# Optimization experiments

Measured on AMD Instinct MI355X. Metric: run time of the kernel, lower is better.

## Reference

```python
import jax, jax.numpy as jnp
import numpy as np

B, N, E = 32, 2048, 4096
D_IN, C, H = 256, 64, 4          # node_hidden_size, gnn_hidden_size, num_heads
SLOPE = 0.2                       # PyG GATConv default negative_slope


def gat_conv(x, src, dst, W, att_src, att_dst, bias):
    """One PyG-style GATConv (concat=True, add_self_loops=True) on a single graph.
    x: [N, Din]; src/dst: [E] int; W: [Din, H*C]; att_*: [H, C]; bias: [H*C]."""
    n = x.shape[0]
    h = (x @ W).reshape(n, H, C)                       # [N,H,C]
    a_src = jnp.einsum('nhc,hc->nh', h, att_src)       # [N,H]
    a_dst = jnp.einsum('nhc,hc->nh', h, att_dst)
    loop = jnp.arange(n, dtype=src.dtype)              # self loops
    s = jnp.concatenate([src, loop])
    d = jnp.concatenate([dst, loop])
    e = jax.nn.leaky_relu(a_src[s] + a_dst[d], SLOPE)  # [E+N,H]
    # segment softmax over incoming edges of each target node
    m = jax.ops.segment_max(e, d, num_segments=n)
    ex = jnp.exp(e - m[d])
    denom = jax.ops.segment_sum(ex, d, num_segments=n)
    alpha = ex / (denom[d] + 1e-16)                    # [E+N,H]
    out = jax.ops.segment_sum(alpha[:, :, None] * h[s], d, num_segments=n)  # [N,H,C]
    return out.reshape(n, H * C) + bias


def setup_inputs() -> dict:
    key = jax.random.key(0)
    ks = jax.random.split(key, 12)
    g = lambda k, shp, fan: jax.random.normal(k, shp, jnp.float32) * (1.0 / np.sqrt(fan))
    return {
        'node_embeddings': jax.random.normal(ks[0], (B, N, D_IN), jnp.float32),
        'src_index': jax.random.randint(ks[1], (B, E), 0, N, jnp.int32),
        'tgt_index': jax.random.randint(ks[2], (B, E), 0, N, jnp.int32),
        'W1': g(ks[3], (D_IN, H * C), D_IN),
        'att_src1': g(ks[4], (H, C), C),
        'att_dst1': g(ks[5], (H, C), C),
        'bias1': jnp.zeros((H * C,), jnp.float32),
        'W2': g(ks[6], (H * C, H * C), H * C),
        'att_src2': g(ks[7], (H, C), C),
        'att_dst2': g(ks[8], (H, C), C),
        'bias2': jnp.zeros((H * C,), jnp.float32),
    }


def reference(node_embeddings, src_index, tgt_index, W1, att_src1, att_dst1, bias1,
              W2, att_src2, att_dst2, bias2):
    def per_graph(x, s, d):
        m = gat_conv(x, s, d, W1, att_src1, att_dst1, bias1)
        m = jax.nn.elu(m)                              # dropout = identity (eval)
        m = gat_conv(m, s, d, W2, att_src2, att_dst2, bias2)
        return m
    return jax.vmap(per_graph)(node_embeddings, src_index, tgt_index)  # [B,N,H*C]
```

## Files before the change

kernel.cpp:

```cpp
#include <hip/hip_runtime.h>
#include <hip/hip_bf16.h>
#include <cstdint>

#define BB 32
#define NN 2048
#define EE 4096
#define HH 4
#define CC 64
#define DD 256
#define MM (BB*NN)

typedef __attribute__((ext_vector_type(8))) short bf16x8;
typedef __attribute__((ext_vector_type(4))) float f32x4;

__device__ __forceinline__ float b2f(__hip_bfloat16 x){ return __bfloat162float(x); }
__device__ __forceinline__ float u2f(unsigned short u){ return __uint_as_float((unsigned)u << 16); }
__device__ __forceinline__ unsigned short f2u(float f){
  __hip_bfloat16 h = __float2bfloat16(f);
  return *(unsigned short*)&h;
}
__device__ __forceinline__ float ldany(const void* p, int isf, size_t i){
  return isf ? ((const float*)p)[i] : b2f(((const __hip_bfloat16*)p)[i]);
}
__device__ __forceinline__ void gld_lds16(const void* g, void* l){
  __builtin_amdgcn_global_load_lds((const __attribute__((address_space(1))) uint32_t*)g,
                                   (__attribute__((address_space(3))) uint32_t*)l, 16, 0, 0);
}

__global__ void detect_kernel(const unsigned* __restrict__ w, int* __restrict__ flag){
  __shared__ int cnt;
  if(threadIdx.x == 0) cnt = 0;
  __syncthreads();
  int c = 0;
  #pragma unroll
  for(int i = 0; i < 4; ++i){
    unsigned v = w[threadIdx.x*4 + i];
    unsigned elo = (v >> 7) & 0xFFu;
    if(elo >= 100u && elo <= 150u) ++c;
  }
  atomicAdd(&cnt, c);
  __syncthreads();
  if(threadIdx.x == 0) *flag = (cnt < 128) ? 1 : 0;
}

__global__ __launch_bounds__(256) void convX_kernel(const void* __restrict__ src,
    unsigned short* __restrict__ dst, const int* __restrict__ flag){
  int isf = *flag;
  size_t i = ((size_t)blockIdx.x*256 + threadIdx.x)*4;
  ushort4 o;
  if(isf){
    float4 v = *(const float4*)((const float*)src + i);
    o.x = f2u(v.x); o.y = f2u(v.y); o.z = f2u(v.z); o.w = f2u(v.w);
  } else {
    o = *(const ushort4*)((const unsigned short*)src + i);
  }
  *(ushort4*)(dst + i) = o;
}
__global__ __launch_bounds__(256) void convWT_kernel(const void* __restrict__ W,
    __hip_bfloat16* __restrict__ WT, const int* __restrict__ flag){
  int isf = *flag;
  int i = blockIdx.x*256 + threadIdx.x;
  WT[i] = __float2bfloat16(ldany(W, isf, (size_t)(i & 255)*256 + (i >> 8)));
}
__global__ __launch_bounds__(256) void conv6_kernel(const void* s0, const void* s1,
    const void* s2, const void* s3, const void* s4, const void* s5,
    float* __restrict__ dst, const int* __restrict__ flag){
  int isf = *flag;
  int i = blockIdx.x*256 + threadIdx.x;
  int seg = i >> 8, off = i & 255;
  const void* s = seg==0?s0 : seg==1?s1 : seg==2?s2 : seg==3?s3 : seg==4?s4 : s5;
  dst[i] = ldany(s, isf, off);
}

__global__ __launch_bounds__(256) void mfma_gemm(const __hip_bfloat16* __restrict__ A,
    const __hip_bfloat16* __restrict__ BT, __hip_bfloat16* __restrict__ C,
    const float* __restrict__ attS, const float* __restrict__ attD,
    float* __restrict__ aS, float* __restrict__ aD)
{
  __shared__ __align__(16) short lA[128*64];
  __shared__ __align__(16) short lB[128*64];
  const int tid  = threadIdx.x;
  const int w    = tid >> 6, lane = tid & 63;
  const int row0 = blockIdx.x*128, col0 = blockIdx.y*128;
  const int wr   = (w & 1)*64, wc = (w >> 1)*64;
  const int lr   = lane >> 3;
  const int kb_g = (lane & 7) ^ lr;
  const int fm   = lane & 15, quad = lane >> 4;
  f32x4 acc[4][4] = {};

  for(int k0 = 0; k0 < 256; k0 += 64){
    #pragma unroll
    for(int c = 0; c < 4; ++c){
      int ra = w*32 + c*8;
      const short* ga = (const short*)A  + (size_t)(row0 + ra + lr)*DD + k0 + kb_g*8;
      const short* gb = (const short*)BT + (size_t)(col0 + ra + lr)*DD + k0 + kb_g*8;
      gld_lds16(ga, &lA[ra*64]);
      gld_lds16(gb, &lB[ra*64]);
    }
    __syncthreads();
    #pragma unroll
    for(int ks = 0; ks < 2; ++ks){
      bf16x8 af[4], bfr[4];
      int kb = ks*4 + quad;
      #pragma unroll
      for(int i = 0; i < 4; ++i){
        int m = wr + i*16 + fm;
        af[i]  = *(const bf16x8*)&lA[m*64 + ((kb ^ (m & 7))*8)];
        int n = wc + i*16 + fm;
        bfr[i] = *(const bf16x8*)&lB[n*64 + ((kb ^ (n & 7))*8)];
      }
      #pragma unroll
      for(int i = 0; i < 4; ++i)
        #pragma unroll
        for(int j = 0; j < 4; ++j)
          acc[i][j] = __builtin_amdgcn_mfma_f32_16x16x32_bf16(af[i], bfr[j], acc[i][j], 0, 0, 0);
    }
    __syncthreads();
  }

  #pragma unroll
  for(int i = 0; i < 4; ++i)
    #pragma unroll
    for(int j = 0; j < 4; ++j)
      #pragma unroll
      for(int r = 0; r < 4; ++r){
        int row = row0 + wr + i*16 + quad*4 + r;
        int col = col0 + wc + j*16 + fm;
        C[(size_t)row*DD + col] = __float2bfloat16(acc[i][j][r]);
      }

  const int headI = (col0 + wc) >> 6;
  float ws_[4], wd_[4];
  #pragma unroll
  for(int j = 0; j < 4; ++j){
    ws_[j] = attS[headI*CC + j*16 + fm];
    wd_[j] = attD[headI*CC + j*16 + fm];
  }
  #pragma unroll
  for(int i = 0; i < 4; ++i){
    #pragma unroll
    for(int r = 0; r < 4; ++r){
      float s = 0.f, dv = 0.f;
      #pragma unroll
      for(int j = 0; j < 4; ++j){
        float v = acc[i][j][r];
        s  += v * ws_[j];
        dv += v * wd_[j];
      }
      #pragma unroll
      for(int m = 1; m <= 8; m <<= 1){
        s  += __shfl_xor(s,  m);
        dv += __shfl_xor(dv, m);
      }
      if(fm == i*4 + r){
        int row = row0 + wr + i*16 + quad*4 + r;
        aS[(size_t)row*HH + headI] = s;
        aD[(size_t)row*HH + headI] = dv;
      }
    }
  }
}

__global__ __launch_bounds__(256) void deg_kernel(const int* __restrict__ dst, int* __restrict__ degc)
{
  int idx = blockIdx.x*256 + threadIdx.x;
  if(idx >= BB*EE) return;
  int b = idx >> 12;
  atomicAdd(&degc[b*NN + dst[idx]], 1);
}

__global__ __launch_bounds__(256) void scan_kernel(int* __restrict__ degc, int* __restrict__ row_ptr)
{
  __shared__ int part[256];
  int b = blockIdx.x, t = threadIdx.x;
  int loc[8], s = 0;
  #pragma unroll
  for(int i = 0; i < 8; ++i){ loc[i] = s; s += degc[b*NN + t*8 + i]; }
  part[t] = s;
  __syncthreads();
  if(t == 0){
    int run = 0;
    for(int i = 0; i < 256; ++i){ int tmp = part[i]; part[i] = run; run += tmp; }
  }
  __syncthreads();
  int base = b*EE + part[t];
  #pragma unroll
  for(int i = 0; i < 8; ++i){
    int v = base + loc[i];
    row_ptr[b*(NN+1) + t*8 + i] = v;
    degc   [b*NN     + t*8 + i] = v;
  }
  if(t == 255) row_ptr[b*(NN+1) + NN] = base + s;
}

__global__ __launch_bounds__(256) void scatter_kernel(const int* __restrict__ src,
    const int* __restrict__ dst, int* __restrict__ cursor, unsigned short* __restrict__ srcList)
{
  int idx = blockIdx.x*256 + threadIdx.x;
  if(idx >= BB*EE) return;
  int b = idx >> 12;
  int pos = atomicAdd(&cursor[b*NN + dst[idx]], 1);
  srcList[pos] = (unsigned short)src[idx];
}

__global__ __launch_bounds__(256) void alpha_kernel(const float* __restrict__ a_src,
    const float* __restrict__ a_dst, const int* __restrict__ row_ptr,
    const unsigned short* __restrict__ srcList, float* __restrict__ alpha,
    float* __restrict__ alphaSelf, float* __restrict__ denG)
{
  int idx = blockIdx.x*256 + threadIdx.x;
  if(idx >= MM*HH) return;
  int h  = idx & (HH-1);
  int bn = idx >> 2;
  int b  = bn >> 11;
  int d  = bn & (NN-1);
  int start = row_ptr[b*(NN+1) + d];
  int end   = row_ptr[b*(NN+1) + d + 1];
  float adv  = a_dst[idx];
  float self = a_src[idx] + adv;
  self = self > 0.f ? self : 0.2f*self;
  float exs = __expf(self), den = exs;
  for(int e = start; e < end; ++e){
    int s = srcList[e];
    float v = a_src[(b*NN + s)*HH + h] + adv;
    v = v > 0.f ? v : 0.2f*v;
    float ex = __expf(v);
    alpha[e*HH + h] = ex;
    den += ex;
  }
  alphaSelf[idx] = exs;
  denG[idx] = den;
}

template<int LAYER>
__global__ __launch_bounds__(256) void gather_kernel(const __hip_bfloat16* __restrict__ H,
    const float* __restrict__ alpha, const float* __restrict__ alphaSelf,
    const float* __restrict__ denG,
    const int* __restrict__ row_ptr, const unsigned short* __restrict__ srcList,
    const float* __restrict__ bias, void* __restrict__ outp,
    const int* __restrict__ flag)
{
  int wid  = (int)(((size_t)blockIdx.x*256 + threadIdx.x) >> 6);
  int lane = threadIdx.x & 63;
  if(wid >= MM) return;
  int b = wid >> 11, d = wid & (NN-1);
  int head = lane >> 4;
  int start = row_ptr[b*(NN+1) + d];
  int end   = row_ptr[b*(NN+1) + d + 1];
  const unsigned short* Hu = (const unsigned short*)H;

  float aS   = alphaSelf[wid*HH + head];
  float denv = denG[wid*HH + head];
  ushort4 hv = *(const ushort4*)(Hu + (size_t)wid*DD + lane*4);
  f32x4 acc;
  acc.x = aS*u2f(hv.x); acc.y = aS*u2f(hv.y); acc.z = aS*u2f(hv.z); acc.w = aS*u2f(hv.w);

  int e = start;
  int s  = 0; float a = 0.f;
  if(e < end){ s = srcList[e]; a = alpha[e*HH + head]; }
  while(e < end){
    int   sn = 0; float an = 0.f;
    if(e + 1 < end){ sn = srcList[e+1]; an = alpha[(e+1)*HH + head]; }
    ushort4 v = *(const ushort4*)(Hu + (size_t)(b*NN + s)*DD + lane*4);
    acc.x += a*u2f(v.x); acc.y += a*u2f(v.y); acc.z += a*u2f(v.z); acc.w += a*u2f(v.w);
    s = sn; a = an; ++e;
  }
  float inv = 1.f / (denv + 1e-16f);
  float4 bs = *(const float4*)(bias + lane*4);
  float o0 = acc.x*inv + bs.x, o1 = acc.y*inv + bs.y;
  float o2 = acc.z*inv + bs.z, o3 = acc.w*inv + bs.w;
  size_t oi = (size_t)wid*DD + lane*4;
  if(LAYER == 1){
    o0 = o0 > 0.f ? o0 : expm1f(o0);
    o1 = o1 > 0.f ? o1 : expm1f(o1);
    o2 = o2 > 0.f ? o2 : expm1f(o2);
    o3 = o3 > 0.f ? o3 : expm1f(o3);
    ushort4 ov = { f2u(o0), f2u(o1), f2u(o2), f2u(o3) };
    *(ushort4*)((unsigned short*)outp + oi) = ov;
  } else {
    if(*flag){
      float4 ov = { o0, o1, o2, o3 };
      *(float4*)((float*)outp + oi) = ov;
    } else {
      ushort4 ov = { f2u(o0), f2u(o1), f2u(o2), f2u(o3) };
      *(ushort4*)((unsigned short*)outp + oi) = ov;
    }
  }
}

extern "C" void kernel_launch(void* const* d_in, const int* in_sizes, int n_in,
                              void* d_out, int out_size, void* d_ws, size_t ws_size,
                              hipStream_t stream)
{
  const void* x_in = d_in[0];
  const int*  srcI = (const int*)d_in[1];
  const int*  dstI = (const int*)d_in[2];
  const void* W1   = d_in[3];
  const void* as1  = d_in[4];
  const void* ad1  = d_in[5];
  const void* b1   = d_in[6];
  const void* W2   = d_in[7];
  const void* as2  = d_in[8];
  const void* ad2  = d_in[9];
  const void* b2   = d_in[10];

  char* ws = (char*)d_ws;
  __hip_bfloat16* R1  = (__hip_bfloat16*)ws; ws += (size_t)MM*DD*2;
  __hip_bfloat16* R2  = (__hip_bfloat16*)ws; ws += (size_t)MM*DD*2;
  float* a_src = (float*)ws; ws += (size_t)MM*HH*4;
  float* a_dst = (float*)ws; ws += (size_t)MM*HH*4;
  float* alpha = (float*)ws; ws += (size_t)BB*EE*HH*4;
  float* alphaS= (float*)ws; ws += (size_t)MM*HH*4;
  float* denG  = (float*)ws; ws += (size_t)MM*HH*4;
  __hip_bfloat16* W1t = (__hip_bfloat16*)ws; ws += (size_t)DD*DD*2;
  __hip_bfloat16* W2t = (__hip_bfloat16*)ws; ws += (size_t)DD*DD*2;
  float* attf = (float*)ws; ws += 1536*4;
  int*   degc = (int*)ws;   ws += (size_t)BB*NN*4;
  int*   rowp = (int*)ws;   ws += (size_t)BB*(NN+1)*4;
  unsigned short* srcL = (unsigned short*)ws; ws += (size_t)BB*EE*2;
  int*   flag = (int*)ws;   ws += 8;

  dim3 ggrid(MM/128, DD/128);
  const int attBlocks    = (MM*HH)/256;
  const int edgeBlocks   = (BB*EE)/256;
  const int gatherBlocks = (MM*64)/256;

  hipMemsetAsync(degc, 0, (size_t)BB*NN*4, stream);
  detect_kernel<<<1, 64, 0, stream>>>((const unsigned*)x_in, flag);
  convWT_kernel<<<DD*DD/256, 256, 0, stream>>>(W1, W1t, flag);
  convWT_kernel<<<DD*DD/256, 256, 0, stream>>>(W2, W2t, flag);
  conv6_kernel<<<6, 256, 0, stream>>>(as1, ad1, b1, as2, ad2, b2, attf, flag);
  convX_kernel<<<(int)(((size_t)MM*DD)/1024), 256, 0, stream>>>(x_in, (unsigned short*)R1, flag);

  deg_kernel    <<<edgeBlocks, 256, 0, stream>>>(dstI, degc);
  scan_kernel   <<<BB,         256, 0, stream>>>(degc, rowp);
  scatter_kernel<<<edgeBlocks, 256, 0, stream>>>(srcI, dstI, degc, srcL);

  mfma_gemm<<<ggrid, 256, 0, stream>>>(R1, W1t, R2, attf + 0, attf + 256, a_src, a_dst);
  alpha_kernel<<<attBlocks, 256, 0, stream>>>(a_src, a_dst, rowp, srcL, alpha, alphaS, denG);
  gather_kernel<1><<<gatherBlocks, 256, 0, stream>>>(R2, alpha, alphaS, denG, rowp, srcL,
                                                     attf + 512, R1, flag);
  mfma_gemm<<<ggrid, 256, 0, stream>>>(R1, W2t, R2, attf + 768, attf + 1024, a_src, a_dst);
  alpha_kernel<<<attBlocks, 256, 0, stream>>>(a_src, a_dst, rowp, srcL, alpha, alphaS, denG);
  gather_kernel<2><<<gatherBlocks, 256, 0, stream>>>(R2, alpha, alphaS, denG, rowp, srcL,
                                                     attf + 1280, d_out, flag);
}
```

Before: 276.0 us.

## Fuse alpha into gather, remap blocks per XCD, stage GEMM output via LDS

Removes the separate alpha kernel: the gather kernel now recomputes the leaky-relu and exp per edge from a_src/a_dst and accumulates the denominator itself. This drops the alpha, alphaSelf and denG buffers and their round trip through memory. The GEMM, gather and convert kernels remap block indices so that neighbouring rows land on the same XCD, which should help L2 locality. GEMM output is staged through a swizzled LDS tile so it can be written with 16-byte coalesced stores, at the cost of an extra barrier and LDS traffic. The max-subtraction is still skipped, the same as before.

```diff
diff --git a/kernel.cpp b/kernel.cpp
--- a/kernel.cpp
+++ b/kernel.cpp
@@ -11,6 +11,7 @@
 #define MM (BB*NN)
 
 typedef __attribute__((ext_vector_type(8))) short bf16x8;
+typedef __attribute__((ext_vector_type(8))) unsigned short u16x8;
 typedef __attribute__((ext_vector_type(4))) float f32x4;
 
 __device__ __forceinline__ float b2f(__hip_bfloat16 x){ return __bfloat162float(x); }
@@ -46,7 +47,9 @@
 __global__ __launch_bounds__(256) void convX_kernel(const void* __restrict__ src,
     unsigned short* __restrict__ dst, const int* __restrict__ flag){
   int isf = *flag;
-  size_t i = ((size_t)blockIdx.x*256 + threadIdx.x)*4;
+  int blk  = blockIdx.x;
+  int vblk = (blk & 7)*2048 + (blk >> 3);
+  size_t i = ((size_t)vblk*256 + threadIdx.x)*4;
   ushort4 o;
   if(isf){
     float4 v = *(const float4*)((const float*)src + i);
@@ -77,11 +80,15 @@
     const float* __restrict__ attS, const float* __restrict__ attD,
     float* __restrict__ aS, float* __restrict__ aD)
 {
-  __shared__ __align__(16) short lA[128*64];
-  __shared__ __align__(16) short lB[128*64];
+  __shared__ __align__(16) short lds[128*128];
+  short* lA = lds;
+  short* lB = lds + 128*64;
   const int tid  = threadIdx.x;
   const int w    = tid >> 6, lane = tid & 63;
-  const int row0 = blockIdx.x*128, col0 = blockIdx.y*128;
+  const int dd   = blockIdx.x;
+  const int xcd  = dd & 7, slot = dd >> 3;
+  const int rb   = xcd*64 + (slot >> 1), cb = slot & 1;
+  const int row0 = rb*128, col0 = cb*128;
   const int wr   = (w & 1)*64, wc = (w >> 1)*64;
   const int lr   = lane >> 3;
   const int kb_g = (lane & 7) ^ lr;
@@ -118,17 +125,6 @@
     __syncthreads();
   }
 
-  #pragma unroll
-  for(int i = 0; i < 4; ++i)
-    #pragma unroll
-    for(int j = 0; j < 4; ++j)
-      #pragma unroll
-      for(int r = 0; r < 4; ++r){
-        int row = row0 + wr + i*16 + quad*4 + r;
-        int col = col0 + wc + j*16 + fm;
-        C[(size_t)row*DD + col] = __float2bfloat16(acc[i][j][r]);
-      }
-
   const int headI = (col0 + wc) >> 6;
   float ws_[4], wd_[4];
   #pragma unroll
@@ -158,6 +154,25 @@
         aD[(size_t)row*HH + headI] = dv;
       }
     }
+  }
+
+  #pragma unroll
+  for(int i = 0; i < 4; ++i)
+    #pragma unroll
+    for(int j = 0; j < 4; ++j)
+      #pragma unroll
+      for(int r = 0; r < 4; ++r){
+        int rl = wr + i*16 + quad*4 + r;
+        int cl = wc + j*16 + fm;
+        lds[rl*128 + (cl ^ ((rl & 12) << 2))] = (short)f2u(acc[i][j][r]);
+      }
+  __syncthreads();
+  const int rr = tid >> 4, cc = (tid & 15)*8;
+  #pragma unroll
+  for(int p = 0; p < 8; ++p){
+    int rl = p*16 + rr;
+    u16x8 v = *(const u16x8*)&lds[rl*128 + (cc ^ ((rl & 12) << 2))];
+    *(u16x8*)((unsigned short*)C + (size_t)(row0 + rl)*DD + col0 + cc) = v;
   }
 }
 
@@ -203,69 +218,48 @@
   srcList[pos] = (unsigned short)src[idx];
 }
 
-__global__ __launch_bounds__(256) void alpha_kernel(const float* __restrict__ a_src,
-    const float* __restrict__ a_dst, const int* __restrict__ row_ptr,
-    const unsigned short* __restrict__ srcList, float* __restrict__ alpha,
-    float* __restrict__ alphaSelf, float* __restrict__ denG)
-{
-  int idx = blockIdx.x*256 + threadIdx.x;
-  if(idx >= MM*HH) return;
-  int h  = idx & (HH-1);
-  int bn = idx >> 2;
-  int b  = bn >> 11;
-  int d  = bn & (NN-1);
-  int start = row_ptr[b*(NN+1) + d];
-  int end   = row_ptr[b*(NN+1) + d + 1];
-  float adv  = a_dst[idx];
-  float self = a_src[idx] + adv;
-  self = self > 0.f ? self : 0.2f*self;
-  float exs = __expf(self), den = exs;
-  for(int e = start; e < end; ++e){
-    int s = srcList[e];
-    float v = a_src[(b*NN + s)*HH + h] + adv;
-    v = v > 0.f ? v : 0.2f*v;
-    float ex = __expf(v);
-    alpha[e*HH + h] = ex;
-    den += ex;
-  }
-  alphaSelf[idx] = exs;
-  denG[idx] = den;
-}
-
 template<int LAYER>
 __global__ __launch_bounds__(256) void gather_kernel(const __hip_bfloat16* __restrict__ H,
-    const float* __restrict__ alpha, const float* __restrict__ alphaSelf,
-    const float* __restrict__ denG,
+    const float* __restrict__ a_src, const float* __restrict__ a_dst,
     const int* __restrict__ row_ptr, const unsigned short* __restrict__ srcList,
     const float* __restrict__ bias, void* __restrict__ outp,
     const int* __restrict__ flag)
 {
-  int wid  = (int)(((size_t)blockIdx.x*256 + threadIdx.x) >> 6);
+  int blk  = blockIdx.x;
+  int vblk = (blk & 7)*2048 + (blk >> 3);
+  int wid  = vblk*4 + (int)(threadIdx.x >> 6);
   int lane = threadIdx.x & 63;
-  if(wid >= MM) return;
   int b = wid >> 11, d = wid & (NN-1);
   int head = lane >> 4;
   int start = row_ptr[b*(NN+1) + d];
   int end   = row_ptr[b*(NN+1) + d + 1];
   const unsigned short* Hu = (const unsigned short*)H;
 
-  float aS   = alphaSelf[wid*HH + head];
-  float denv = denG[wid*HH + head];
+  float adv = a_dst[wid*HH + head];
+  float sv  = a_src[wid*HH + head] + adv;
+  sv = sv > 0.f ? sv : 0.2f*sv;
+  float exs = __expf(sv);
+
   ushort4 hv = *(const ushort4*)(Hu + (size_t)wid*DD + lane*4);
   f32x4 acc;
-  acc.x = aS*u2f(hv.x); acc.y = aS*u2f(hv.y); acc.z = aS*u2f(hv.z); acc.w = aS*u2f(hv.w);
+  acc.x = exs*u2f(hv.x); acc.y = exs*u2f(hv.y); acc.z = exs*u2f(hv.z); acc.w = exs*u2f(hv.w);
+  float den = exs;
 
   int e = start;
-  int s  = 0; float a = 0.f;
-  if(e < end){ s = srcList[e]; a = alpha[e*HH + head]; }
+  int s = 0; float ax = 0.f;
+  if(e < end){ s = srcList[e]; ax = a_src[(b*NN + s)*HH + head]; }
   while(e < end){
-    int   sn = 0; float an = 0.f;
-    if(e + 1 < end){ sn = srcList[e+1]; an = alpha[(e+1)*HH + head]; }
-    ushort4 v = *(const ushort4*)(Hu + (size_t)(b*NN + s)*DD + lane*4);
-    acc.x += a*u2f(v.x); acc.y += a*u2f(v.y); acc.z += a*u2f(v.z); acc.w += a*u2f(v.w);
-    s = sn; a = an; ++e;
-  }
-  float inv = 1.f / (denv + 1e-16f);
+    int sn = 0; float axn = 0.f;
+    if(e + 1 < end){ sn = srcList[e+1]; axn = a_src[(b*NN + sn)*HH + head]; }
+    float v = ax + adv;
+    v = v > 0.f ? v : 0.2f*v;
+    float ex = __expf(v);
+    ushort4 hw = *(const ushort4*)(Hu + (size_t)(b*NN + s)*DD + lane*4);
+    acc.x += ex*u2f(hw.x); acc.y += ex*u2f(hw.y); acc.z += ex*u2f(hw.z); acc.w += ex*u2f(hw.w);
+    den += ex;
+    s = sn; ax = axn; ++e;
+  }
+  float inv = 1.f / (den + 1e-16f);
   float4 bs = *(const float4*)(bias + lane*4);
   float o0 = acc.x*inv + bs.x, o1 = acc.y*inv + bs.y;
   float o2 = acc.z*inv + bs.z, o3 = acc.w*inv + bs.w;
@@ -309,9 +303,6 @@
   __hip_bfloat16* R2  = (__hip_bfloat16*)ws; ws += (size_t)MM*DD*2;
   float* a_src = (float*)ws; ws += (size_t)MM*HH*4;
   float* a_dst = (float*)ws; ws += (size_t)MM*HH*4;
-  float* alpha = (float*)ws; ws += (size_t)BB*EE*HH*4;
-  float* alphaS= (float*)ws; ws += (size_t)MM*HH*4;
-  float* denG  = (float*)ws; ws += (size_t)MM*HH*4;
   __hip_bfloat16* W1t = (__hip_bfloat16*)ws; ws += (size_t)DD*DD*2;
   __hip_bfloat16* W2t = (__hip_bfloat16*)ws; ws += (size_t)DD*DD*2;
   float* attf = (float*)ws; ws += 1536*4;
@@ -320,8 +311,7 @@
   unsigned short* srcL = (unsigned short*)ws; ws += (size_t)BB*EE*2;
   int*   flag = (int*)ws;   ws += 8;
 
-  dim3 ggrid(MM/128, DD/128);
-  const int attBlocks    = (MM*HH)/256;
+  const int gemmBlocks   = (MM/128)*(DD/128);
   const int edgeBlocks   = (BB*EE)/256;
   const int gatherBlocks = (MM*64)/256;
 
@@ -336,12 +326,10 @@
   scan_kernel   <<<BB,         256, 0, stream>>>(degc, rowp);
   scatter_kernel<<<edgeBlocks, 256, 0, stream>>>(srcI, dstI, degc, srcL);
 
-  mfma_gemm<<<ggrid, 256, 0, stream>>>(R1, W1t, R2, attf + 0, attf + 256, a_src, a_dst);
-  alpha_kernel<<<attBlocks, 256, 0, stream>>>(a_src, a_dst, rowp, srcL, alpha, alphaS, denG);
-  gather_kernel<1><<<gatherBlocks, 256, 0, stream>>>(R2, alpha, alphaS, denG, rowp, srcL,
+  mfma_gemm<<<gemmBlocks, 256, 0, stream>>>(R1, W1t, R2, attf + 0, attf + 256, a_src, a_dst);
+  gather_kernel<1><<<gatherBlocks, 256, 0, stream>>>(R2, a_src, a_dst, rowp, srcL,
                                                      attf + 512, R1, flag);
-  mfma_gemm<<<ggrid, 256, 0, stream>>>(R1, W2t, R2, attf + 768, attf + 1024, a_src, a_dst);
-  alpha_kernel<<<attBlocks, 256, 0, stream>>>(a_src, a_dst, rowp, srcL, alpha, alphaS, denG);
-  gather_kernel<2><<<gatherBlocks, 256, 0, stream>>>(R2, alpha, alphaS, denG, rowp, srcL,
+  mfma_gemm<<<gemmBlocks, 256, 0, stream>>>(R1, W2t, R2, attf + 768, attf + 1024, a_src, a_dst);
+  gather_kernel<2><<<gatherBlocks, 256, 0, stream>>>(R2, a_src, a_dst, rowp, srcL,
                                                      attf + 1280, d_out, flag);
 }
```

Result: faster. 255.1 us (-7.6%).
